# Kernel optimization log

Measured on AMD Instinct MI355X. Metric: run time of the kernel, lower is better.

The kernel has to match this reference:

```python
import jax, jax.numpy as jnp
import numpy as np

DIM_IN = 512
HIDDEN = 512
DIM_OUT = 512
BATCH = 256

def _n_tri(d):
    return (d * d + d) // 2

def _quad_expand(x):
    # x: [B, D] -> [B, D + (D^2+D)/2] with upper-triu (incl diag) pairwise products
    d = x.shape[1]
    iu0, iu1 = np.triu_indices(d)  # static indices
    x_sq = x[:, iu0] * x[:, iu1]  # [B, n_tri] -- avoids materializing full outer
    return jnp.concatenate([x, x_sq], axis=-1)

def setup_inputs() -> dict:
    key = jax.random.key(0)
    k = jax.random.split(key, 5)
    f0 = DIM_IN + _n_tri(DIM_IN)
    f1 = HIDDEN + _n_tri(HIDDEN)
    s0 = 1.0 / np.sqrt(f0)
    s1 = 1.0 / np.sqrt(f1)
    return {
        "x": jax.random.normal(k[0], (BATCH, DIM_IN), dtype=jnp.float32),
        "W0": jax.random.uniform(k[1], (HIDDEN, f0), dtype=jnp.float32, minval=-s0, maxval=s0),
        "b0": jax.random.uniform(k[2], (HIDDEN,), dtype=jnp.float32, minval=-s0, maxval=s0),
        "W1": jax.random.uniform(k[3], (DIM_OUT, f1), dtype=jnp.float32, minval=-s1, maxval=s1),
        "b1": jax.random.uniform(k[4], (DIM_OUT,), dtype=jnp.float32, minval=-s1, maxval=s1),
    }

def reference(x, W0, b0, W1, b1):
    h = _quad_expand(x) @ W0.T + b0  # [B, HIDDEN]
    out = _quad_expand(h) @ W1.T + b1  # [B, DIM_OUT]
    return out
```

## Files before the change

### kernel.cpp

```cpp
#include <hip/hip_runtime.h>

typedef short s16x8 __attribute__((ext_vector_type(8)));
typedef float f32x4 __attribute__((ext_vector_type(4)));

#define DIM     512
#define BATCH   256
#define NTRI    131328
#define FDIM    131840
#define KBLOCKS 2060
#define BN      64
#define NTILES  8
#define CCH     64

__device__ __forceinline__ unsigned short f2bf(float f) {
  __bf16 h = (__bf16)f;
  return __builtin_bit_cast(unsigned short, h);
}
__device__ __forceinline__ float bf2f(unsigned short s) {
  union { unsigned u; float f; } v; v.u = (unsigned)s << 16; return v.f;
}
__device__ __forceinline__ unsigned pk2(float a, float b) {
  return (unsigned)f2bf(a) | ((unsigned)f2bf(b) << 16);
}
__device__ __forceinline__ int swz(int m) { return (m ^ (m >> 2)) & 7; }

__device__ __forceinline__ void dma16(const void* g, void* l) {
  __builtin_amdgcn_global_load_lds(
      (const __attribute__((address_space(1))) void*)g,
      (__attribute__((address_space(3))) void*)l, 16, 0, 0);
}

__global__ void build_table(unsigned* __restrict__ table) {
  int i = blockIdx.x;
  int base = i * DIM - (i * (i - 1)) / 2;
  int len = DIM - i;
  for (int t = threadIdx.x; t < len; t += blockDim.x)
    table[base + t] = ((unsigned)i << 16) | (unsigned)(i + t);
}

__global__ void transpose_x(const float* __restrict__ x, unsigned short* __restrict__ Xt) {
  int t = blockIdx.x * blockDim.x + threadIdx.x;
  int r = t & (BATCH - 1);
  int c = t >> 8;
  Xt[c * BATCH + r] = f2bf(x[r * DIM + c]);
}

__global__ __launch_bounds__(512)
void featgen(const unsigned* __restrict__ table,
             const unsigned short* __restrict__ Xt,
             uint4* __restrict__ Feat)
{
  __shared__ uint4 img[2048];
  const int kb = blockIdx.x;
  const int tid = threadIdx.x;
  const int s8 = tid >> 6;
  const int lane = tid & 63;
  const int f0 = kb * 64 + s8 * 8;

  if (f0 < DIM) {
    #pragma unroll
    for (int mb = 0; mb < 4; ++mb) {
      int m = mb * 64 + lane;
      unsigned short v[8];
      #pragma unroll
      for (int e = 0; e < 8; ++e) v[e] = Xt[(f0 + e) * BATCH + m];
      uint4 pk;
      pk.x = (unsigned)v[0] | ((unsigned)v[1] << 16);
      pk.y = (unsigned)v[2] | ((unsigned)v[3] << 16);
      pk.z = (unsigned)v[4] | ((unsigned)v[5] << 16);
      pk.w = (unsigned)v[6] | ((unsigned)v[7] << 16);
      img[m * 8 + (s8 ^ swz(m))] = pk;
    }
  } else {
    int p0 = f0 - DIM;
    unsigned t0 = table[p0], t7 = table[p0 + 7];
    if ((t0 >> 16) == (t7 >> 16)) {
      int i = (int)(t0 >> 16), j0 = (int)(t0 & 0xffffu);
      #pragma unroll
      for (int mb = 0; mb < 4; ++mb) {
        int m = mb * 64 + lane;
        float xi = bf2f(Xt[i * BATCH + m]);
        float pr[8];
        #pragma unroll
        for (int e = 0; e < 8; ++e) pr[e] = xi * bf2f(Xt[(j0 + e) * BATCH + m]);
        uint4 pk = make_uint4(pk2(pr[0], pr[1]), pk2(pr[2], pr[3]),
                              pk2(pr[4], pr[5]), pk2(pr[6], pr[7]));
        img[m * 8 + (s8 ^ swz(m))] = pk;
      }
    } else {
      unsigned tt[8];
      #pragma unroll
      for (int e = 0; e < 8; ++e) tt[e] = table[p0 + e];
      #pragma unroll
      for (int mb = 0; mb < 4; ++mb) {
        int m = mb * 64 + lane;
        float pr[8];
        #pragma unroll
        for (int e = 0; e < 8; ++e)
          pr[e] = bf2f(Xt[(tt[e] >> 16) * BATCH + m]) * bf2f(Xt[(tt[e] & 0xffffu) * BATCH + m]);
        uint4 pk = make_uint4(pk2(pr[0], pr[1]), pk2(pr[2], pr[3]),
                              pk2(pr[4], pr[5]), pk2(pr[6], pr[7]));
        img[m * 8 + (s8 ^ swz(m))] = pk;
      }
    }
  }
  __syncthreads();
  uint4* out = Feat + (size_t)kb * 2048;
  #pragma unroll
  for (int p = 0; p < 4; ++p) out[p * 512 + tid] = img[p * 512 + tid];
}

__global__ __launch_bounds__(512, 4)
void qgemm(const uint4* __restrict__ Feat,
           const float* __restrict__ W,
           float* __restrict__ partial,
           int C)
{
  __shared__ unsigned short As[2 * BATCH * 64];
  __shared__ unsigned short Ws[2 * 64 * 64];
  const int chunk = blockIdx.x % C;
  const int ntile = blockIdx.x / C;
  const int kb0 = (KBLOCKS * chunk) / C;
  const int kb1 = (KBLOCKS * (chunk + 1)) / C;
  const int n0 = ntile * BN;
  const int tid = threadIdx.x;
  const int lane = tid & 63;
  const int wave = tid >> 6;
  const int wm = wave & 3;
  const int wn = wave >> 2;
  const int lm = lane & 15;
  const int lk = lane >> 4;

  const int wr0 = tid >> 4;
  const int wc16 = tid & 15;

  f32x4 acc[4][2] = {};
  f32x4 wregC[2], wregN[2];

  const char* fsrc0 = (const char*)Feat + tid * 16;
  char* adst0 = (char*)As + tid * 16;
  const float* wp0 = W + (size_t)(n0 + wr0) * FDIM + wc16 * 4;
  const size_t wrow32 = (size_t)32 * FDIM;

  {
    const char* src = fsrc0 + (size_t)kb0 * 32768;
    #pragma unroll
    for (int p = 0; p < 4; ++p) dma16(src + p * 8192, adst0 + p * 8192);
    #pragma unroll
    for (int it = 0; it < 2; ++it)
      wregC[it] = *(const f32x4*)(wp0 + it * wrow32 + (size_t)kb0 * 64);
  }

  for (int kb = kb0; kb < kb1 - 1; ++kb) {
    const int pc = (kb - kb0) & 1;
    {
      const char* src = fsrc0 + (size_t)(kb + 1) * 32768;
      char* dst = adst0 + (pc ^ 1) * 32768;
      #pragma unroll
      for (int p = 0; p < 4; ++p) dma16(src + p * 8192, dst + p * 8192);
      #pragma unroll
      for (int it = 0; it < 2; ++it)
        wregN[it] = *(const f32x4*)(wp0 + it * wrow32 + (size_t)(kb + 1) * 64);
    }
    __builtin_amdgcn_sched_barrier(0);
    #pragma unroll
    for (int it = 0; it < 2; ++it) {
      int r = wr0 + it * 32;
      int slot = (wc16 >> 1) ^ swz(r);
      *(uint2*)((char*)Ws + pc * 8192 + r * 128 + slot * 16 + (wc16 & 1) * 8) =
          make_uint2(pk2(wregC[it][0], wregC[it][1]), pk2(wregC[it][2], wregC[it][3]));
    }
    asm volatile("s_waitcnt lgkmcnt(0)" ::: "memory");
    __builtin_amdgcn_sched_barrier(0);
    __builtin_amdgcn_s_barrier();
    {
      const char* asb = (const char*)As + pc * 32768;
      const char* wsb = (const char*)Ws + pc * 8192;
      #pragma unroll
      for (int ks = 0; ks < 2; ++ks) {
        s16x8 bfr[2], afr[4];
        #pragma unroll
        for (int nf = 0; nf < 2; ++nf) {
          int n = wn * 32 + nf * 16 + lm;
          int slot = (ks * 4 + lk) ^ swz(n);
          bfr[nf] = *(const s16x8*)(wsb + n * 128 + slot * 16);
        }
        #pragma unroll
        for (int mf = 0; mf < 4; ++mf) {
          int mm = wm * 64 + mf * 16 + lm;
          int slot = (ks * 4 + lk) ^ swz(mm);
          afr[mf] = *(const s16x8*)(asb + mm * 128 + slot * 16);
        }
        #pragma unroll
        for (int mf = 0; mf < 4; ++mf)
          #pragma unroll
          for (int nf = 0; nf < 2; ++nf)
            acc[mf][nf] = __builtin_amdgcn_mfma_f32_16x16x32_bf16(afr[mf], bfr[nf], acc[mf][nf], 0, 0, 0);
      }
    }
    __builtin_amdgcn_s_barrier();
    wregC[0] = wregN[0]; wregC[1] = wregN[1];
  }

  {
    const int pc = (kb1 - 1 - kb0) & 1;
    #pragma unroll
    for (int it = 0; it < 2; ++it) {
      int r = wr0 + it * 32;
      int slot = (wc16 >> 1) ^ swz(r);
      *(uint2*)((char*)Ws + pc * 8192 + r * 128 + slot * 16 + (wc16 & 1) * 8) =
          make_uint2(pk2(wregC[it][0], wregC[it][1]), pk2(wregC[it][2], wregC[it][3]));
    }
    asm volatile("s_waitcnt lgkmcnt(0)" ::: "memory");
    __builtin_amdgcn_s_barrier();
    const char* asb = (const char*)As + pc * 32768;
    const char* wsb = (const char*)Ws + pc * 8192;
    #pragma unroll
    for (int ks = 0; ks < 2; ++ks) {
      s16x8 bfr[2], afr[4];
      #pragma unroll
      for (int nf = 0; nf < 2; ++nf) {
        int n = wn * 32 + nf * 16 + lm;
        int slot = (ks * 4 + lk) ^ swz(n);
        bfr[nf] = *(const s16x8*)(wsb + n * 128 + slot * 16);
      }
      #pragma unroll
      for (int mf = 0; mf < 4; ++mf) {
        int mm = wm * 64 + mf * 16 + lm;
        int slot = (ks * 4 + lk) ^ swz(mm);
        afr[mf] = *(const s16x8*)(asb + mm * 128 + slot * 16);
      }
      #pragma unroll
      for (int mf = 0; mf < 4; ++mf)
        #pragma unroll
        for (int nf = 0; nf < 2; ++nf)
          acc[mf][nf] = __builtin_amdgcn_mfma_f32_16x16x32_bf16(afr[mf], bfr[nf], acc[mf][nf], 0, 0, 0);
    }
  }

  float* pout = partial + (size_t)chunk * (BATCH * DIM);
  #pragma unroll
  for (int mf = 0; mf < 4; ++mf) {
    #pragma unroll
    for (int nf = 0; nf < 2; ++nf) {
      int mrow = wm * 64 + mf * 16 + lk * 4;
      int ncol = n0 + wn * 32 + nf * 16 + lm;
      #pragma unroll
      for (int r = 0; r < 4; ++r)
        pout[(size_t)(mrow + r) * DIM + ncol] = acc[mf][nf][r];
    }
  }
}

__global__ void reduce_h(const float* __restrict__ partial, const float* __restrict__ bias,
                         unsigned short* __restrict__ Ht, int C) {
  int t = blockIdx.x * blockDim.x + threadIdx.x;
  int b = t >> 9;
  int o = t & (DIM - 1);
  float s = bias[o];
  #pragma unroll 4
  for (int c = 0; c < C; ++c) s += partial[(size_t)c * (BATCH * DIM) + t];
  Ht[o * BATCH + b] = f2bf(s);
}

__global__ void reduce_out(const float* __restrict__ partial, const float* __restrict__ bias,
                           float* __restrict__ out, int C) {
  int t = blockIdx.x * blockDim.x + threadIdx.x;
  int o = t & (DIM - 1);
  float s = bias[o];
  #pragma unroll 4
  for (int c = 0; c < C; ++c) s += partial[(size_t)c * (BATCH * DIM) + t];
  out[t] = s;
}

extern "C" void kernel_launch(void* const* d_in, const int* in_sizes, int n_in,
                              void* d_out, int out_size, void* d_ws, size_t ws_size,
                              hipStream_t stream) {
  const float* x  = (const float*)d_in[0];
  const float* W0 = (const float*)d_in[1];
  const float* b0 = (const float*)d_in[2];
  const float* W1 = (const float*)d_in[3];
  const float* b1 = (const float*)d_in[4];
  float* out = (float*)d_out;

  char* ws = (char*)d_ws;
  unsigned* table    = (unsigned*)ws;
  unsigned short* Xt = (unsigned short*)(ws + 525312);
  unsigned short* Ht = (unsigned short*)(ws + 787456);
  uint4* Feat        = (uint4*)(ws + 1049600);
  size_t feat_end    = 1049600 + (size_t)KBLOCKS * 32768;
  float* partial     = (float*)(ws + feat_end);

  size_t avail = (ws_size > feat_end) ? (ws_size - feat_end) : 0;
  int C = (int)(avail / ((size_t)BATCH * DIM * sizeof(float)));
  if (C > CCH) C = CCH;
  if (C < 1)  C = 1;

  build_table<<<dim3(512), dim3(256), 0, stream>>>(table);
  transpose_x<<<dim3(512), dim3(256), 0, stream>>>(x, Xt);

  featgen<<<dim3(KBLOCKS), dim3(512), 0, stream>>>(table, Xt, Feat);
  qgemm<<<dim3(NTILES * C), dim3(512), 0, stream>>>(Feat, W0, partial, C);
  reduce_h<<<dim3(512), dim3(256), 0, stream>>>(partial, b0, Ht, C);

  featgen<<<dim3(KBLOCKS), dim3(512), 0, stream>>>(table, Ht, Feat);
  qgemm<<<dim3(NTILES * C), dim3(512), 0, stream>>>(Feat, W1, partial, C);
  reduce_out<<<dim3(512), dim3(256), 0, stream>>>(partial, b1, out, C);
}
```

Measured before the change: 232.3 us.

## Store split-K partials as bf16, vectorize reductions, fuse setup kernels, prioritize MFMA

Split-K partial sums are now written as bf16 rather than fp32, which halves the partial write and read traffic. The reduce kernels now read 8 values at a time with uint4 loads and launch fewer blocks. The table-build and transpose kernels are merged into one launch, and the MFMA inner loop now issues all LDS fragment loads before the MFMAs, with s_setprio raising wave priority during the MFMA phase. The cost is lower precision in the partials: up to 64 bf16-rounded chunks are summed, so accuracy drops. The reduce kernels also run with far less parallelism.

```diff
diff --git a/kernel.cpp b/kernel.cpp
--- a/kernel.cpp
+++ b/kernel.cpp
@@ -30,19 +30,21 @@
       (__attribute__((address_space(3))) void*)l, 16, 0, 0);
 }
 
-__global__ void build_table(unsigned* __restrict__ table) {
-  int i = blockIdx.x;
-  int base = i * DIM - (i * (i - 1)) / 2;
-  int len = DIM - i;
-  for (int t = threadIdx.x; t < len; t += blockDim.x)
-    table[base + t] = ((unsigned)i << 16) | (unsigned)(i + t);
-}
-
-__global__ void transpose_x(const float* __restrict__ x, unsigned short* __restrict__ Xt) {
-  int t = blockIdx.x * blockDim.x + threadIdx.x;
-  int r = t & (BATCH - 1);
-  int c = t >> 8;
-  Xt[c * BATCH + r] = f2bf(x[r * DIM + c]);
+__global__ void setup(unsigned* __restrict__ table, const float* __restrict__ x,
+                      unsigned short* __restrict__ Xt) {
+  int bid = blockIdx.x;
+  if (bid < 512) {
+    int i = bid;
+    int base = i * DIM - (i * (i - 1)) / 2;
+    int len = DIM - i;
+    for (int t = threadIdx.x; t < len; t += blockDim.x)
+      table[base + t] = ((unsigned)i << 16) | (unsigned)(i + t);
+  } else {
+    int t = (bid - 512) * blockDim.x + threadIdx.x;
+    int r = t & (BATCH - 1);
+    int c = t >> 8;
+    Xt[c * BATCH + r] = f2bf(x[r * DIM + c]);
+  }
 }
 
 __global__ __launch_bounds__(512)
@@ -113,7 +115,7 @@
 __global__ __launch_bounds__(512, 4)
 void qgemm(const uint4* __restrict__ Feat,
            const float* __restrict__ W,
-           float* __restrict__ partial,
+           unsigned short* __restrict__ partial,
            int C)
 {
   __shared__ unsigned short As[2 * BATCH * 64];
@@ -176,27 +178,31 @@
     {
       const char* asb = (const char*)As + pc * 32768;
       const char* wsb = (const char*)Ws + pc * 8192;
+      s16x8 bfr[2][2], afr[2][4];
       #pragma unroll
       for (int ks = 0; ks < 2; ++ks) {
-        s16x8 bfr[2], afr[4];
         #pragma unroll
         for (int nf = 0; nf < 2; ++nf) {
           int n = wn * 32 + nf * 16 + lm;
           int slot = (ks * 4 + lk) ^ swz(n);
-          bfr[nf] = *(const s16x8*)(wsb + n * 128 + slot * 16);
+          bfr[ks][nf] = *(const s16x8*)(wsb + n * 128 + slot * 16);
         }
         #pragma unroll
         for (int mf = 0; mf < 4; ++mf) {
           int mm = wm * 64 + mf * 16 + lm;
           int slot = (ks * 4 + lk) ^ swz(mm);
-          afr[mf] = *(const s16x8*)(asb + mm * 128 + slot * 16);
+          afr[ks][mf] = *(const s16x8*)(asb + mm * 128 + slot * 16);
         }
+      }
+      __builtin_amdgcn_s_setprio(1);
+      #pragma unroll
+      for (int ks = 0; ks < 2; ++ks)
         #pragma unroll
         for (int mf = 0; mf < 4; ++mf)
           #pragma unroll
           for (int nf = 0; nf < 2; ++nf)
-            acc[mf][nf] = __builtin_amdgcn_mfma_f32_16x16x32_bf16(afr[mf], bfr[nf], acc[mf][nf], 0, 0, 0);
-      }
+            acc[mf][nf] = __builtin_amdgcn_mfma_f32_16x16x32_bf16(afr[ks][mf], bfr[ks][nf], acc[mf][nf], 0, 0, 0);
+      __builtin_amdgcn_s_setprio(0);
     }
     __builtin_amdgcn_s_barrier();
     wregC[0] = wregN[0]; wregC[1] = wregN[1];
@@ -215,30 +221,32 @@
     __builtin_amdgcn_s_barrier();
     const char* asb = (const char*)As + pc * 32768;
     const char* wsb = (const char*)Ws + pc * 8192;
+    s16x8 bfr[2][2], afr[2][4];
     #pragma unroll
     for (int ks = 0; ks < 2; ++ks) {
-      s16x8 bfr[2], afr[4];
       #pragma unroll
       for (int nf = 0; nf < 2; ++nf) {
         int n = wn * 32 + nf * 16 + lm;
         int slot = (ks * 4 + lk) ^ swz(n);
-        bfr[nf] = *(const s16x8*)(wsb + n * 128 + slot * 16);
+        bfr[ks][nf] = *(const s16x8*)(wsb + n * 128 + slot * 16);
       }
       #pragma unroll
       for (int mf = 0; mf < 4; ++mf) {
         int mm = wm * 64 + mf * 16 + lm;
         int slot = (ks * 4 + lk) ^ swz(mm);
-        afr[mf] = *(const s16x8*)(asb + mm * 128 + slot * 16);
-      }
+        afr[ks][mf] = *(const s16x8*)(asb + mm * 128 + slot * 16);
+      }
+    }
+    #pragma unroll
+    for (int ks = 0; ks < 2; ++ks)
       #pragma unroll
       for (int mf = 0; mf < 4; ++mf)
         #pragma unroll
         for (int nf = 0; nf < 2; ++nf)
-          acc[mf][nf] = __builtin_amdgcn_mfma_f32_16x16x32_bf16(afr[mf], bfr[nf], acc[mf][nf], 0, 0, 0);
-    }
-  }
-
-  float* pout = partial + (size_t)chunk * (BATCH * DIM);
+          acc[mf][nf] = __builtin_amdgcn_mfma_f32_16x16x32_bf16(afr[ks][mf], bfr[ks][nf], acc[mf][nf], 0, 0, 0);
+  }
+
+  unsigned short* pout = partial + (size_t)chunk * (BATCH * DIM);
   #pragma unroll
   for (int mf = 0; mf < 4; ++mf) {
     #pragma unroll
@@ -247,30 +255,55 @@
       int ncol = n0 + wn * 32 + nf * 16 + lm;
       #pragma unroll
       for (int r = 0; r < 4; ++r)
-        pout[(size_t)(mrow + r) * DIM + ncol] = acc[mf][nf][r];
-    }
-  }
-}
-
-__global__ void reduce_h(const float* __restrict__ partial, const float* __restrict__ bias,
+        pout[(size_t)(mrow + r) * DIM + ncol] = f2bf(acc[mf][nf][r]);
+    }
+  }
+}
+
+__global__ void reduce_h(const unsigned short* __restrict__ partial, const float* __restrict__ bias,
                          unsigned short* __restrict__ Ht, int C) {
-  int t = blockIdx.x * blockDim.x + threadIdx.x;
-  int b = t >> 9;
-  int o = t & (DIM - 1);
-  float s = bias[o];
-  #pragma unroll 4
-  for (int c = 0; c < C; ++c) s += partial[(size_t)c * (BATCH * DIM) + t];
-  Ht[o * BATCH + b] = f2bf(s);
-}
-
-__global__ void reduce_out(const float* __restrict__ partial, const float* __restrict__ bias,
+  int u = blockIdx.x * blockDim.x + threadIdx.x;
+  int t8 = u * 8;
+  int b = t8 >> 9;
+  int o0 = t8 & (DIM - 1);
+  float s[8];
+  #pragma unroll
+  for (int e = 0; e < 8; ++e) s[e] = bias[o0 + e];
+  for (int c = 0; c < C; ++c) {
+    uint4 v = *(const uint4*)(partial + (size_t)c * (BATCH * DIM) + t8);
+    unsigned w[4] = {v.x, v.y, v.z, v.w};
+    #pragma unroll
+    for (int p = 0; p < 4; ++p) {
+      s[2*p]   += bf2f((unsigned short)(w[p] & 0xffffu));
+      s[2*p+1] += bf2f((unsigned short)(w[p] >> 16));
+    }
+  }
+  #pragma unroll
+  for (int e = 0; e < 8; ++e)
+    Ht[(o0 + e) * BATCH + b] = f2bf(s[e]);
+}
+
+__global__ void reduce_out(const unsigned short* __restrict__ partial, const float* __restrict__ bias,
                            float* __restrict__ out, int C) {
-  int t = blockIdx.x * blockDim.x + threadIdx.x;
-  int o = t & (DIM - 1);
-  float s = bias[o];
-  #pragma unroll 4
-  for (int c = 0; c < C; ++c) s += partial[(size_t)c * (BATCH * DIM) + t];
-  out[t] = s;
+  int u = blockIdx.x * blockDim.x + threadIdx.x;
+  int t8 = u * 8;
+  int o0 = t8 & (DIM - 1);
+  float s[8];
+  #pragma unroll
+  for (int e = 0; e < 8; ++e) s[e] = bias[o0 + e];
+  for (int c = 0; c < C; ++c) {
+    uint4 v = *(const uint4*)(partial + (size_t)c * (BATCH * DIM) + t8);
+    unsigned w[4] = {v.x, v.y, v.z, v.w};
+    #pragma unroll
+    for (int p = 0; p < 4; ++p) {
+      s[2*p]   += bf2f((unsigned short)(w[p] & 0xffffu));
+      s[2*p+1] += bf2f((unsigned short)(w[p] >> 16));
+    }
+  }
+  f32x4 lo = {s[0], s[1], s[2], s[3]};
+  f32x4 hi = {s[4], s[5], s[6], s[7]};
+  *(f32x4*)(out + t8) = lo;
+  *(f32x4*)(out + t8 + 4) = hi;
 }
 
 extern "C" void kernel_launch(void* const* d_in, const int* in_sizes, int n_in,
@@ -289,21 +322,20 @@
   unsigned short* Ht = (unsigned short*)(ws + 787456);
   uint4* Feat        = (uint4*)(ws + 1049600);
   size_t feat_end    = 1049600 + (size_t)KBLOCKS * 32768;
-  float* partial     = (float*)(ws + feat_end);
+  unsigned short* partial = (unsigned short*)(ws + feat_end);
 
   size_t avail = (ws_size > feat_end) ? (ws_size - feat_end) : 0;
-  int C = (int)(avail / ((size_t)BATCH * DIM * sizeof(float)));
+  int C = (int)(avail / ((size_t)BATCH * DIM * sizeof(unsigned short)));
   if (C > CCH) C = CCH;
   if (C < 1)  C = 1;
 
-  build_table<<<dim3(512), dim3(256), 0, stream>>>(table);
-  transpose_x<<<dim3(512), dim3(256), 0, stream>>>(x, Xt);
+  setup<<<dim3(1024), dim3(256), 0, stream>>>(table, x, Xt);
 
   featgen<<<dim3(KBLOCKS), dim3(512), 0, stream>>>(table, Xt, Feat);
   qgemm<<<dim3(NTILES * C), dim3(512), 0, stream>>>(Feat, W0, partial, C);
-  reduce_h<<<dim3(512), dim3(256), 0, stream>>>(partial, b0, Ht, C);
+  reduce_h<<<dim3(64), dim3(256), 0, stream>>>(partial, b0, Ht, C);
 
   featgen<<<dim3(KBLOCKS), dim3(512), 0, stream>>>(table, Ht, Feat);
   qgemm<<<dim3(NTILES * C), dim3(512), 0, stream>>>(Feat, W1, partial, C);
-  reduce_out<<<dim3(512), dim3(256), 0, stream>>>(partial, b1, out, C);
-}
+  reduce_out<<<dim3(64), dim3(256), 0, stream>>>(partial, b1, out, C);
+}
```

Result: slower. 238.3 us (+2.6%).
